# Optimization experiments

Hardware: AMD Instinct MI355X
Metric: run time of the kernel (lower is better)

The kernel has to match this reference:

```python
import jax, jax.numpy as jnp
import numpy as np

B, S, D, H, DH = 8192, 64, 32, 4, 8

def setup_inputs() -> dict:
    key = jax.random.key(0)
    ks = jax.random.split(key, 10)
    lim = 1.0 / np.sqrt(D)
    def lin(k):
        kw, kb = jax.random.split(k)
        W = jax.random.uniform(kw, (D, D), jnp.float32, -lim, lim)
        b = jax.random.uniform(kb, (D,), jnp.float32, -lim, lim)
        return W, b
    Wq, bq = lin(ks[0]); Wk, bk = lin(ks[1]); Wv, bv = lin(ks[2]); Wp, bp = lin(ks[3])
    x = jax.random.normal(ks[4], (B, S, D), jnp.float32)
    always_attend_upto = jax.random.randint(ks[5], (B,), 0, 64, jnp.int64 if jax.config.jax_enable_x64 else jnp.int32)
    return {"x": x, "always_attend_upto": always_attend_upto,
            "Wq": Wq, "bq": bq, "Wk": Wk, "bk": bk, "Wv": Wv, "bv": bv, "Wp": Wp, "bp": bp}

def reference(x, always_attend_upto, Wq, bq, Wk, bk, Wv, bv, Wp, bp):
    # QKV projections (torch Linear: y = x @ W.T + b)
    def heads(W, b):
        y = x @ W.T + b                      # [B,S,D]
        return y.reshape(B, S, H, DH).transpose(0, 2, 1, 3)  # [B,H,S,DH]
    q, k, v = heads(Wq, bq), heads(Wk, bk), heads(Wv, bv)
    score = jnp.einsum('bhqd,bhkd->bhqk', q, k) / jnp.sqrt(jnp.float32(DH))
    # prefix-LM mask: allowed if causal (j<=i) OR key in prefix (j < length[b])
    i = jnp.arange(S)[:, None]
    j = jnp.arange(S)[None, :]
    causal = j <= i                                        # [S,S]
    prefix = j[None, :, :] < always_attend_upto[:, None, None]  # [B,S,S]
    allowed = (causal[None] | prefix)[:, None, :, :]       # [B,1,S,S]
    score = jnp.where(allowed, score, -jnp.inf)
    attn = jax.nn.softmax(score, axis=-1)
    out = jnp.einsum('bhqk,bhkd->bhqd', attn, v)           # [B,H,S,DH]
    out = out.transpose(0, 2, 1, 3).reshape(B, S, D)
    return out @ Wp.T + bp
```

## Files before the change

kernel.cpp:

```cpp
#include <hip/hip_runtime.h>
#include <cstdint>
#include <cstddef>

#define NB 8192
#define NBPB 4

typedef __attribute__((ext_vector_type(8))) short short8;
typedef __attribute__((ext_vector_type(4))) float f32x4;

union S8U { short8 s; unsigned u[4]; uint4 v; };
union FI { float f; int i; unsigned u; };

static __device__ __forceinline__ unsigned pk2(float a, float b) {
    unsigned short ua = __builtin_bit_cast(unsigned short, (__bf16)a);
    unsigned short ub = __builtin_bit_cast(unsigned short, (__bf16)b);
    return (unsigned)ua | ((unsigned)ub << 16);
}

#define MFMA __builtin_amdgcn_mfma_f32_16x16x32_bf16
#define BPERM __builtin_amdgcn_ds_bpermute

__global__ __launch_bounds__(128, 4) void fused_attn_mfma(
    const float* __restrict__ x,
    const int*   __restrict__ aatt,
    const float* __restrict__ Wq, const float* __restrict__ bq,
    const float* __restrict__ Wk, const float* __restrict__ bk,
    const float* __restrict__ Wv, const float* __restrict__ bv,
    const float* __restrict__ Wp, const float* __restrict__ bp,
    float* __restrict__ out)
{
    __shared__ __align__(16) short klds[64][40];
    __shared__ __align__(16) short vbt[33][72];

    const int tid  = threadIdx.x;
    const int w    = tid >> 6;
    const int lane = tid & 63;
    const int q4   = lane >> 4;
    const int l15  = lane & 15;

    const unsigned bmask = (q4 == 0) ? 0xFFFFFFFFu : 0u;

    auto wrow = [&](const float* W, int row) -> short8 {
        const float* p = W + row*32 + q4*8;
        float4 u0 = *(const float4*)p;
        float4 u1 = *(const float4*)(p + 4);
        S8U t;
        t.u[0] = pk2(u0.x, u0.y); t.u[1] = pk2(u0.z, u0.w);
        t.u[2] = pk2(u1.x, u1.y); t.u[3] = pk2(u1.z, u1.w);
        return t.s;
    };

    const float escale = 0.35355339059327373f * 1.4426950408889634f;

    const short8 wq8 = wrow(Wq, 16*w + l15);
    const short8 wk8 = wrow(Wk, 16*w + l15);
    const short8 wv8 = wrow(Wv, 16*w + l15);
    const float4 bq4 = *(const float4*)(bq + 16*w + q4*4);
    const float4 bk4 = *(const float4*)(bk + 16*w + q4*4);
    const float  bvv = bv[16*w + l15];
    short8 wpb[2];
    wpb[0] = wrow(Wp, l15);
    wpb[1] = wrow(Wp, 16 + l15);
    const float bpv[2] = { bp[l15], bp[16 + l15] };

    if (q4 == 0) {
        uint2 ones; ones.x = 0x3F803F80u; ones.y = 0x3F803F80u;
        *(uint2*)&vbt[32][l15*4] = ones;
    }

#pragma unroll 1
    for (int bi = 0; bi < NBPB; ++bi) {
        const int b = blockIdx.x * NBPB + bi;
        const int aab = aatt[b];

        int cmpv[4];
#pragma unroll
        for (int it = 0; it < 4; ++it) cmpv[it] = max(l15 + 16*it, aab - 1) - q4*4;

        short8 xa[4];
        const float* xb = x + (size_t)b * 64 * 32;
#pragma unroll
        for (int nt = 0; nt < 4; ++nt) {
            const float* p = xb + (nt*16 + l15)*32 + q4*8;
            float4 u0 = *(const float4*)p;
            float4 u1 = *(const float4*)(p + 4);
            S8U t;
            t.u[0] = pk2(u0.x, u0.y); t.u[1] = pk2(u0.z, u0.w);
            t.u[2] = pk2(u1.x, u1.y); t.u[3] = pk2(u1.z, u1.w);
            xa[nt] = t.s;
        }

        unsigned qpk01[4], qpk23[4];
#pragma unroll
        for (int nt = 0; nt < 4; ++nt) {
            f32x4 acc = {0.f,0.f,0.f,0.f};
            acc = MFMA(wq8, xa[nt], acc, 0,0,0);
            qpk01[nt] = pk2((acc[0]+bq4.x)*escale, (acc[1]+bq4.y)*escale);
            qpk23[nt] = pk2((acc[2]+bq4.z)*escale, (acc[3]+bq4.w)*escale);
        }
#pragma unroll
        for (int nt = 0; nt < 4; ++nt) {
            f32x4 acc = {0.f,0.f,0.f,0.f};
            acc = MFMA(wk8, xa[nt], acc, 0,0,0);
            uint2 w2;
            w2.x = pk2(acc[0]+bk4.x, acc[1]+bk4.y);
            w2.y = pk2(acc[2]+bk4.z, acc[3]+bk4.w);
            *(uint2*)&klds[nt*16 + l15][16*w + q4*4] = w2;
        }
#pragma unroll
        for (int mt = 0; mt < 4; ++mt) {
            f32x4 acc = {0.f,0.f,0.f,0.f};
            acc = MFMA(xa[mt], wv8, acc, 0,0,0);
            uint2 w2;
            w2.x = pk2(acc[0]+bvv, acc[1]+bvv);
            w2.y = pk2(acc[2]+bvv, acc[3]+bvv);
            *(uint2*)&vbt[16*w + l15][(mt >> 1)*32 + q4*8 + (mt & 1)*4] = w2;
        }

#pragma unroll
        for (int hl = 0; hl < 2; ++hl) {
            const int idxA = (32*hl + l15) * 4;
            const int idxB = idxA + 64;

            short8 sqb[4];
#pragma unroll
            for (int it = 0; it < 4; ++it) {
                S8U t;
                t.u[0] = (unsigned)BPERM(idxA, (int)qpk01[it]) & bmask;
                t.u[1] = (unsigned)BPERM(idxA, (int)qpk23[it]) & bmask;
                t.u[2] = (unsigned)BPERM(idxB, (int)qpk01[it]) & bmask;
                t.u[3] = (unsigned)BPERM(idxB, (int)qpk23[it]) & bmask;
                sqb[it] = t.s;
            }

            const int avrow = (l15 < 8) ? (16*w + 8*hl + l15) : 32;

            f32x4 oacch[4];
#pragma unroll
            for (int it = 0; it < 4; ++it) oacch[it] = (f32x4){0.f,0.f,0.f,0.f};

#pragma unroll
            for (int jb = 0; jb < 2; ++jb) {
                S8U ska0, ska1, av;
                ska0.v = *(const uint4*)&klds[jb*32 + l15][16*w + 8*hl];
                ska1.v = *(const uint4*)&klds[jb*32 + 16 + l15][16*w + 8*hl];
                av.v   = *(const uint4*)&vbt[avrow][jb*32 + q4*8];

#pragma unroll
                for (int it = 0; it < 4; ++it) {
                    S8U pb;
                    {
                        f32x4 sacc = {0.f,0.f,0.f,0.f};
                        sacc = MFMA(ska0.s, sqb[it], sacc, 0,0,0);
                        float e[4];
#pragma unroll
                        for (int r = 0; r < 4; ++r) {
                            float ee = __builtin_amdgcn_exp2f(sacc[r]);
                            e[r] = (jb*32 + r <= cmpv[it]) ? ee : 0.0f;
                        }
                        pb.u[0] = pk2(e[0], e[1]); pb.u[1] = pk2(e[2], e[3]);
                    }
                    {
                        f32x4 sacc = {0.f,0.f,0.f,0.f};
                        sacc = MFMA(ska1.s, sqb[it], sacc, 0,0,0);
                        float e[4];
#pragma unroll
                        for (int r = 0; r < 4; ++r) {
                            float ee = __builtin_amdgcn_exp2f(sacc[r]);
                            e[r] = (jb*32 + 16 + r <= cmpv[it]) ? ee : 0.0f;
                        }
                        pb.u[2] = pk2(e[0], e[1]); pb.u[3] = pk2(e[2], e[3]);
                    }
                    oacch[it] = MFMA(av.s, pb.s, oacch[it], 0,0,0);
                }
            }

#pragma unroll
            for (int it = 0; it < 4; ++it) {
                FI s; s.i = BPERM((32 + l15) * 4, __builtin_bit_cast(int, oacch[it][0]));
                const float inv = __builtin_amdgcn_rcpf(s.f);
                const unsigned o01 = pk2(oacch[it][0]*inv, oacch[it][1]*inv);
                const unsigned o23 = pk2(oacch[it][2]*inv, oacch[it][3]*inv);
                if (q4 < 2) {
                    uint2 ow; ow.x = o01; ow.y = o23;
                    *(uint2*)&klds[it*16 + l15][(2*w + hl)*8 + q4*4] = ow;
                }
            }
        }

        __syncthreads();

        float* ob = out + (size_t)b * 64 * 32;
#pragma unroll
        for (int u = 0; u < 2; ++u) {
            S8U oa; oa.v = *(const uint4*)&klds[(2*w + u)*16 + l15][q4*8];
#pragma unroll
            for (int nt = 0; nt < 2; ++nt) {
                f32x4 y = {0.f,0.f,0.f,0.f};
                y = MFMA(oa.s, wpb[nt], y, 0,0,0);
#pragma unroll
                for (int r = 0; r < 4; ++r)
                    ob[((2*w + u)*16 + q4*4 + r)*32 + nt*16 + l15] = y[r] + bpv[nt];
            }
        }

        __syncthreads();
    }
}

extern "C" void kernel_launch(void* const* d_in, const int* in_sizes, int n_in,
                              void* d_out, int out_size, void* d_ws, size_t ws_size,
                              hipStream_t stream) {
    const float* x  = (const float*)d_in[0];
    const int*   aa = (const int*)d_in[1];
    const float* Wq = (const float*)d_in[2];
    const float* bq = (const float*)d_in[3];
    const float* Wk = (const float*)d_in[4];
    const float* bk = (const float*)d_in[5];
    const float* Wv = (const float*)d_in[6];
    const float* bv = (const float*)d_in[7];
    const float* Wp = (const float*)d_in[8];
    const float* bp = (const float*)d_in[9];
    float* out = (float*)d_out;

    dim3 grid(NB / NBPB), block(128);
    hipLaunchKernelGGL(fused_attn_mfma, grid, block, 0, stream,
                       x, aa, Wq, bq, Wk, bk, Wv, bv, Wp, bp, out);
}
```

Before: 51.65 us.

## Mask packed bf16 probabilities with precomputed bitmasks and halve batches per block

Replaces the per-element compare-and-select on exp2 results with precomputed 32-bit pair masks ANDed onto the packed bf16 words. This cuts VALU compare/cndmask work in the inner softmax loop. It also halves the number of batches per block, doubling the grid size for more parallelism. The 32 precomputed masks add register pressure, which may lower occupancy.

```diff
diff --git a/kernel.cpp b/kernel.cpp
--- a/kernel.cpp
+++ b/kernel.cpp
@@ -3,7 +3,7 @@
 #include <cstddef>
 
 #define NB 8192
-#define NBPB 4
+#define NBPB 2
 
 typedef __attribute__((ext_vector_type(8))) short short8;
 typedef __attribute__((ext_vector_type(4))) float f32x4;
@@ -68,6 +68,11 @@
         *(uint2*)&vbt[32][l15*4] = ones;
     }
 
+    auto pairmask = [](int s) -> unsigned {
+        unsigned m = (s >= 1) ? 0xFFFFFFFFu : 0x0000FFFFu;
+        return (s < 0) ? 0u : m;
+    };
+
 #pragma unroll 1
     for (int bi = 0; bi < NBPB; ++bi) {
         const int b = blockIdx.x * NBPB + bi;
@@ -76,6 +81,18 @@
         int cmpv[4];
 #pragma unroll
         for (int it = 0; it < 4; ++it) cmpv[it] = max(l15 + 16*it, aab - 1) - q4*4;
+
+        unsigned pm[2][4][4];
+#pragma unroll
+        for (int jb = 0; jb < 2; ++jb)
+#pragma unroll
+            for (int it = 0; it < 4; ++it) {
+                const int t0 = cmpv[it] - jb*32;
+                pm[jb][it][0] = pairmask(t0);
+                pm[jb][it][1] = pairmask(t0 - 2);
+                pm[jb][it][2] = pairmask(t0 - 16);
+                pm[jb][it][3] = pairmask(t0 - 18);
+            }
 
         short8 xa[4];
         const float* xb = x + (size_t)b * 64 * 32;
@@ -152,24 +169,18 @@
                     {
                         f32x4 sacc = {0.f,0.f,0.f,0.f};
                         sacc = MFMA(ska0.s, sqb[it], sacc, 0,0,0);
-                        float e[4];
-#pragma unroll
-                        for (int r = 0; r < 4; ++r) {
-                            float ee = __builtin_amdgcn_exp2f(sacc[r]);
-                            e[r] = (jb*32 + r <= cmpv[it]) ? ee : 0.0f;
-                        }
-                        pb.u[0] = pk2(e[0], e[1]); pb.u[1] = pk2(e[2], e[3]);
+                        pb.u[0] = pk2(__builtin_amdgcn_exp2f(sacc[0]),
+                                      __builtin_amdgcn_exp2f(sacc[1])) & pm[jb][it][0];
+                        pb.u[1] = pk2(__builtin_amdgcn_exp2f(sacc[2]),
+                                      __builtin_amdgcn_exp2f(sacc[3])) & pm[jb][it][1];
                     }
                     {
                         f32x4 sacc = {0.f,0.f,0.f,0.f};
                         sacc = MFMA(ska1.s, sqb[it], sacc, 0,0,0);
-                        float e[4];
-#pragma unroll
-                        for (int r = 0; r < 4; ++r) {
-                            float ee = __builtin_amdgcn_exp2f(sacc[r]);
-                            e[r] = (jb*32 + 16 + r <= cmpv[it]) ? ee : 0.0f;
-                        }
-                        pb.u[2] = pk2(e[0], e[1]); pb.u[3] = pk2(e[2], e[3]);
+                        pb.u[2] = pk2(__builtin_amdgcn_exp2f(sacc[0]),
+                                      __builtin_amdgcn_exp2f(sacc[1])) & pm[jb][it][2];
+                        pb.u[3] = pk2(__builtin_amdgcn_exp2f(sacc[2]),
+                                      __builtin_amdgcn_exp2f(sacc[3])) & pm[jb][it][3];
                     }
                     oacch[it] = MFMA(av.s, pb.s, oacch[it], 0,0,0);
                 }
@@ -177,7 +188,8 @@
 
 #pragma unroll
             for (int it = 0; it < 4; ++it) {
-                FI s; s.i = BPERM((32 + l15) * 4, __builtin_bit_cast(int, oacch[it][0]));
+                FI s; s.i = BPERM((32 + l15) * 4,
+                                  __builtin_bit_cast(int, oacch[it][0]));
                 const float inv = __builtin_amdgcn_rcpf(s.f);
                 const unsigned o01 = pk2(oacch[it][0]*inv, oacch[it][1]*inv);
                 const unsigned o23 = pk2(oacch[it][2]*inv, oacch[it][3]*inv);
```

Measured after the change: 50.76 us. No clear change (-1.7%).
